# Kernel optimization log

Measured on AMD Instinct MI355X. Metric: run time of the kernel, lower is better.

## Reference

```python
import jax, jax.numpy as jnp
import numpy as np

B, T, D = 2, 2048, 1024
H, DK, DV = 16, 64, 64
DFF = 4096
CONV = 4
EPS = 1e-6


def _layernorm(x):
    # elementwise_affine=False LayerNorm
    mu = jnp.mean(x, axis=-1, keepdims=True)
    xc = x - mu
    return xc * jax.lax.rsqrt(jnp.mean(xc * xc, axis=-1, keepdims=True) + EPS)


def _l2norm(x):
    return x * jax.lax.rsqrt(jnp.sum(x * x, axis=-1, keepdims=True) + EPS)


def _modulate(x, shift, scale):
    return x * (1.0 + scale[:, None, :]) + shift[:, None, :]


def _short_conv(x, w):
    # causal depthwise conv1d (kernel CONV) + SiLU; x: [B,T,Dc], w: [Dc,CONV]
    Tn = x.shape[1]
    xp = jnp.pad(x, ((0, 0), (CONV - 1, 0), (0, 0)))
    y = xp[:, 0:Tn, :] * w[:, 0]
    for i in range(1, CONV):
        y = y + xp[:, i:i + Tn, :] * w[:, i]
    return jax.nn.silu(y)


def _delta_rule(q, k, v, beta):
    # delta-rule linear-attention recurrence (fused_recurrent form)
    # q,k: [B,T,H,DK], v: [B,T,H,DV], beta: [B,T,H]
    scale = DK ** -0.5
    qs = jnp.moveaxis(q * scale, 1, 0)
    ks = jnp.moveaxis(k, 1, 0)
    vs = jnp.moveaxis(v, 1, 0)
    bs = jnp.moveaxis(beta, 1, 0)
    S0 = jnp.zeros((q.shape[0], H, DK, DV), q.dtype)

    def step(S, inp):
        qt, kt, vt, bt = inp
        pred = jnp.einsum('bhk,bhkv->bhv', kt, S)        # k_t^T S
        delta = bt[..., None] * (vt - pred)              # beta_t (v_t - k_t^T S)
        S = S + jnp.einsum('bhk,bhv->bhkv', kt, delta)   # rank-1 delta update
        o = jnp.einsum('bhk,bhkv->bhv', qt, S)
        return S, o

    _, o = jax.lax.scan(step, S0, (qs, ks, vs, bs))
    return jnp.moveaxis(o, 0, 1)  # [B,T,H,DV]


def _deltanet(xm, Wq, Wk, Wv, Wb, wcq, wck, wcv, w_onorm, Wo):
    Bb, Tn, Dd = xm.shape
    q = _short_conv(xm @ Wq, wcq)
    k = _short_conv(xm @ Wk, wck)
    v = _short_conv(xm @ Wv, wcv)
    beta = jax.nn.sigmoid(xm @ Wb)                        # [B,T,H]
    q = _l2norm(q.reshape(Bb, Tn, H, DK))
    k = _l2norm(k.reshape(Bb, Tn, H, DK))
    v = v.reshape(Bb, Tn, H, DV)
    o = _delta_rule(q, k, v, beta)
    # per-head RMSNorm output norm
    o = o * jax.lax.rsqrt(jnp.mean(o * o, axis=-1, keepdims=True) + EPS) * w_onorm
    return o.reshape(Bb, Tn, Dd) @ Wo


def setup_inputs():
    key = jax.random.key(0)
    ks = jax.random.split(key, 20)
    s = 0.02
    return {
        "x": jax.random.normal(ks[0], (B, T, D), jnp.float32),
        "c": jax.random.normal(ks[1], (B, D), jnp.float32),
        "W_ada": jax.random.normal(ks[2], (D, 6 * D), jnp.float32) * s,
        "b_ada": jnp.zeros((6 * D,), jnp.float32),
        "Wq": jax.random.normal(ks[3], (D, H * DK), jnp.float32) * s,
        "Wk": jax.random.normal(ks[4], (D, H * DK), jnp.float32) * s,
        "Wv": jax.random.normal(ks[5], (D, H * DV), jnp.float32) * s,
        "Wb": jax.random.normal(ks[6], (D, H), jnp.float32) * s,
        "wcq": jax.random.normal(ks[7], (H * DK, CONV), jnp.float32) * 0.5,
        "wck": jax.random.normal(ks[8], (H * DK, CONV), jnp.float32) * 0.5,
        "wcv": jax.random.normal(ks[9], (H * DV, CONV), jnp.float32) * 0.5,
        "w_onorm": jnp.ones((DV,), jnp.float32),
        "Wo": jax.random.normal(ks[10], (H * DV, D), jnp.float32) * s,
        "W1": jax.random.normal(ks[11], (D, DFF), jnp.float32) * s,
        "b1": jnp.zeros((DFF,), jnp.float32),
        "W2": jax.random.normal(ks[12], (DFF, D), jnp.float32) * s,
        "b2": jnp.zeros((D,), jnp.float32),
    }


def reference(x, c, W_ada, b_ada, Wq, Wk, Wv, Wb, wcq, wck, wcv, w_onorm, Wo, W1, b1, W2, b2):
    mods = jax.nn.silu(c) @ W_ada + b_ada
    sh_a, sc_a, g_a, sh_m, sc_m, g_m = jnp.split(mods, 6, axis=-1)
    attn_out = _deltanet(_modulate(_layernorm(x), sh_a, sc_a),
                         Wq, Wk, Wv, Wb, wcq, wck, wcv, w_onorm, Wo)
    x = x + g_a[:, None, :] * attn_out
    h = _modulate(_layernorm(x), sh_m, sc_m)
    mlp = jax.nn.gelu(h @ W1 + b1, approximate=True) @ W2 + b2
    return x + g_m[:, None, :] * mlp
```

## Files before the change

### kernel.cpp

```cpp
#include <hip/hip_runtime.h>
#include <math.h>

typedef __attribute__((ext_vector_type(4))) float f32x4;
typedef __attribute__((ext_vector_type(8))) short bf16x8;
typedef __attribute__((ext_vector_type(4))) short s16x4;

__device__ __forceinline__ short f2bf(float f) {
  union { float f; unsigned u; } c; c.f = f;
  unsigned r = c.u + 0x7FFFu + ((c.u >> 16) & 1u);
  return (short)(r >> 16);
}
__device__ __forceinline__ float bf2f(short b) {
  union { unsigned u; float f; } c;
  c.u = ((unsigned)(unsigned short)b) << 16;
  return c.f;
}
__device__ __forceinline__ f32x4 mfma16(bf16x8 a, bf16x8 b, f32x4 c) {
  return __builtin_amdgcn_mfma_f32_16x16x32_bf16(a, b, c, 0, 0, 0);
}
__device__ __forceinline__ void gload16(const short* g, short* l) {
  __builtin_amdgcn_global_load_lds(
      (const __attribute__((address_space(1))) unsigned int*)g,
      (__attribute__((address_space(3))) unsigned int*)l, 16, 0, 0);
}

__global__ void k_transpose_bf16(const float* __restrict__ in, short* __restrict__ out,
                                 int K, int N) {
  __shared__ float tile[32][33];
  int n0 = blockIdx.x * 32, k0 = blockIdx.y * 32;
  int tx = threadIdx.x & 31, ty = threadIdx.x >> 5;
  for (int i = ty; i < 32; i += 8) tile[i][tx] = in[(long)(k0 + i) * N + n0 + tx];
  __syncthreads();
  for (int i = ty; i < 32; i += 8) out[(long)(n0 + i) * K + k0 + tx] = f2bf(tile[tx][i]);
}

__global__ void k_transpose_wb(const float* __restrict__ Wb, short* __restrict__ WbT) {
  int idx = blockIdx.x * 256 + threadIdx.x;
  int n = idx >> 10, k = idx & 1023;
  WbT[n * 1024 + k] = f2bf(Wb[k * 16 + n]);
}

__global__ void k_mods_p1(const float* __restrict__ c, const float* __restrict__ W_ada,
                          float* __restrict__ part) {
  int cx = blockIdx.x, dc = blockIdx.y, tid = threadIdx.x;
  __shared__ float s0[128], s1[128];
  if (tid < 128) {
    float v = c[dc * 128 + tid];
    s0[tid] = v / (1.f + expf(-v));
  } else {
    int t = tid - 128;
    float v = c[1024 + dc * 128 + t];
    s1[t] = v / (1.f + expf(-v));
  }
  __syncthreads();
  int col = cx * 256 + tid;
  float a0 = 0.f, a1 = 0.f;
  const float* wp = W_ada + (long)(dc * 128) * 6144 + col;
  for (int d = 0; d < 128; d++) {
    float w = wp[(long)d * 6144];
    a0 += s0[d] * w;
    a1 += s1[d] * w;
  }
  part[((long)dc * 2) * 6144 + col] = a0;
  part[((long)dc * 2 + 1) * 6144 + col] = a1;
}
__global__ void k_mods_p2(const float* __restrict__ part, const float* __restrict__ b_ada,
                          float* __restrict__ mods) {
  int col = blockIdx.x * 256 + threadIdx.x;
  float a0 = 0.f, a1 = 0.f;
  for (int dc = 0; dc < 8; dc++) {
    a0 += part[((long)dc * 2) * 6144 + col];
    a1 += part[((long)dc * 2 + 1) * 6144 + col];
  }
  float b = b_ada[col];
  mods[col] = a0 + b;
  mods[6144 + col] = a1 + b;
}

__global__ void k_ln_mod(const float* __restrict__ x, const float* __restrict__ mods,
                         short* __restrict__ out, int sh_off, int sc_off) {
  int row = blockIdx.x, tid = threadIdx.x, b = row >> 11;
  float4 v = ((const float4*)(x + (long)row * 1024))[tid];
  float s = v.x + v.y + v.z + v.w;
  float ss = v.x * v.x + v.y * v.y + v.z * v.z + v.w * v.w;
  #pragma unroll
  for (int off = 1; off < 64; off <<= 1) { s += __shfl_xor(s, off); ss += __shfl_xor(ss, off); }
  __shared__ float rs[4], rq[4];
  if ((tid & 63) == 0) { rs[tid >> 6] = s; rq[tid >> 6] = ss; }
  __syncthreads();
  s = rs[0] + rs[1] + rs[2] + rs[3];
  ss = rq[0] + rq[1] + rq[2] + rq[3];
  float mu = s * (1.f / 1024.f);
  float rstd = rsqrtf(ss * (1.f / 1024.f) - mu * mu + 1e-6f);
  const float* shv = mods + b * 6144 + sh_off;
  const float* scv = mods + b * 6144 + sc_off;
  int c0 = tid * 4;
  float xs[4] = {v.x, v.y, v.z, v.w};
  s16x4 ov;
  #pragma unroll
  for (int j = 0; j < 4; j++)
    ov[j] = f2bf((xs[j] - mu) * rstd * (1.f + scv[c0 + j]) + shv[c0 + j]);
  ((s16x4*)(out + (long)row * 1024))[tid] = ov;
}

__global__ __launch_bounds__(256) void k_beta_mfma(
    const short* __restrict__ xm, const short* __restrict__ WbT,
    float* __restrict__ beta) {
  int tid = threadIdx.x, w = tid >> 6, l = tid & 63;
  int lr = l & 15, lg = l >> 4;
  int row0 = blockIdx.x * 64 + w * 16;
  const short* ap = xm + (long)(row0 + lr) * 1024 + lg * 8;
  const short* bp = WbT + lr * 1024 + lg * 8;
  f32x4 acc = (f32x4){0.f, 0.f, 0.f, 0.f};
  #pragma unroll 8
  for (int kk = 0; kk < 1024; kk += 32) {
    bf16x8 a = *(const bf16x8*)(ap + kk);
    bf16x8 b = *(const bf16x8*)(bp + kk);
    acc = mfma16(a, b, acc);
  }
  #pragma unroll
  for (int i = 0; i < 4; i++) {
    int row = row0 + lg * 4 + i;
    beta[row * 16 + lr] = 1.f / (1.f + expf(-acc[i]));
  }
}

template <int NORM, int OUTBF>
__global__ void k_conv(const float* __restrict__ pre, const float* __restrict__ w,
                       void* __restrict__ out, float scale, int ldp) {
  int row = blockIdx.x, tid = threadIdx.x, t = row & 2047;
  int c0 = tid * 4;
  const float* base = pre + (long)row * ldp + c0;
  float xr[4][4];
  #pragma unroll
  for (int i = 0; i < 4; i++) {
    int tt = t - 3 + i;
    if (tt >= 0) {
      float4 xv = *(const float4*)(base + (long)(i - 3) * ldp);
      xr[i][0] = xv.x; xr[i][1] = xv.y; xr[i][2] = xv.z; xr[i][3] = xv.w;
    } else {
      xr[i][0] = xr[i][1] = xr[i][2] = xr[i][3] = 0.f;
    }
  }
  float y[4];
  #pragma unroll
  for (int j = 0; j < 4; j++) {
    float4 wv = *(const float4*)(w + (long)(c0 + j) * 4);
    float a = xr[0][j] * wv.x + xr[1][j] * wv.y + xr[2][j] * wv.z + xr[3][j] * wv.w;
    y[j] = a / (1.f + expf(-a));
  }
  if (NORM) {
    float ssq = y[0] * y[0] + y[1] * y[1] + y[2] * y[2] + y[3] * y[3];
    #pragma unroll
    for (int off = 1; off < 16; off <<= 1) ssq += __shfl_xor(ssq, off);
    float r = rsqrtf(ssq + 1e-6f) * scale;
    #pragma unroll
    for (int j = 0; j < 4; j++) y[j] *= r;
  }
  if (OUTBF) {
    s16x4 ov;
    #pragma unroll
    for (int j = 0; j < 4; j++) ov[j] = f2bf(y[j]);
    ((s16x4*)((short*)out + (long)row * 1024))[tid] = ov;
  } else {
    float4 ov = {y[0], y[1], y[2], y[3]};
    ((float4*)((float*)out + (long)row * 1024))[tid] = ov;
  }
}

__global__ __launch_bounds__(256) void k_phaseA(
    const float* __restrict__ kf, const float* __restrict__ vf,
    const short* __restrict__ qbf, const float* __restrict__ beta,
    short* __restrict__ Wc, short* __restrict__ UTc,
    short* __restrict__ Lc, short* __restrict__ KTc) {
  int chunk = blockIdx.x, chain = blockIdx.y;
  int b = chain >> 4, h = chain & 15;
  long rowbase = (long)b * 2048 + chunk * 64;
  int col0 = h * 64;
  long cb = ((long)chain * 32 + chunk) * 4096;
  __shared__ short Kb[64][72], KTb[64][72], VTb[64][72], Mb[64][72];
  __shared__ float Sf[64][65], Mf[64][65];
  __shared__ float Tl[4][16][20];
  __shared__ float bl[64];
  int tid = threadIdx.x, w = tid >> 6, l = tid & 63;
  int lr = l & 15, lg = l >> 4;

  for (int i = tid; i < 64 * 65; i += 256) (&Mf[0][0])[i] = 0.f;
  {
    int t = tid & 63, g = tid >> 6;
    if (tid < 64) bl[tid] = beta[(rowbase + tid) * 16 + h];
    #pragma unroll
    for (int i = 0; i < 4; i++) {
      int dk = g * 16 + i * 4;
      float4 kv = *(const float4*)(kf + (rowbase + t) * 1024 + col0 + dk);
      float4 vv = *(const float4*)(vf + (rowbase + t) * 1024 + col0 + dk);
      #pragma unroll
      for (int j = 0; j < 4; j++) {
        short ks = f2bf(((const float*)&kv)[j]);
        Kb[t][dk + j] = ks;
        KTb[dk + j][t] = ks;
        VTb[dk + j][t] = f2bf(((const float*)&vv)[j]);
      }
    }
  }
  __syncthreads();
  {
    bf16x8 af0 = *(const bf16x8*)&Kb[w * 16 + lr][lg * 8];
    bf16x8 af1 = *(const bf16x8*)&Kb[w * 16 + lr][32 + lg * 8];
    #pragma unroll
    for (int nt = 0; nt < 4; nt++) {
      f32x4 acc = (f32x4){0.f, 0.f, 0.f, 0.f};
      acc = mfma16(af0, *(const bf16x8*)&Kb[nt * 16 + lr][lg * 8], acc);
      acc = mfma16(af1, *(const bf16x8*)&Kb[nt * 16 + lr][32 + lg * 8], acc);
      #pragma unroll
      for (int i = 0; i < 4; i++) {
        int row = w * 16 + lg * 4 + i, col = nt * 16 + lr;
        Sf[row][col] = (col < row) ? bl[row] * acc[i] : 0.f;
      }
    }
  }
  __syncthreads();
  if (w == 0) {
    int blk = l >> 4, colc = l & 15, base = blk * 16;
    float mcol[16];
    #pragma unroll
    for (int r = 0; r < 16; r++) {
      float s = (r == colc) ? 1.f : 0.f;
      #pragma unroll
      for (int j = 0; j < 16; j++)
        if (j < r) s -= Sf[base + r][base + j] * mcol[j];
      mcol[r] = s;
    }
    #pragma unroll
    for (int r = 0; r < 16; r++) Mf[base + r][base + colc] = mcol[r];
  } else if (w <= 2) {
    int idx = (w - 1) * 64 + l;
    #pragma unroll
    for (int i = 0; i < 4; i++) {
      int v = idx * 4 + i, row = v >> 3, cg = (v & 7) * 8;
      *(bf16x8*)&KTc[cb + row * 64 + cg] = *(const bf16x8*)&KTb[row][cg];
    }
  }
  __syncthreads();
  if (w < 3) {
    int j = w;
    int r = l & 15, c4 = (l >> 4) * 4;
    for (int i = j + 1; i < 4; i++) {
      float t4[4] = {0.f, 0.f, 0.f, 0.f};
      for (int k = j; k < i; k++) {
        #pragma unroll
        for (int m = 0; m < 16; m++) {
          float a = Sf[i * 16 + r][k * 16 + m];
          #pragma unroll
          for (int ii = 0; ii < 4; ii++)
            t4[ii] += a * Mf[k * 16 + m][j * 16 + c4 + ii];
        }
      }
      #pragma unroll
      for (int ii = 0; ii < 4; ii++) Tl[w][r][c4 + ii] = t4[ii];
      float o4[4] = {0.f, 0.f, 0.f, 0.f};
      #pragma unroll
      for (int m = 0; m < 16; m++) {
        float d = Mf[i * 16 + r][i * 16 + m];
        #pragma unroll
        for (int ii = 0; ii < 4; ii++) o4[ii] += d * Tl[w][m][c4 + ii];
      }
      #pragma unroll
      for (int ii = 0; ii < 4; ii++) Mf[i * 16 + r][j * 16 + c4 + ii] = -o4[ii];
    }
  }
  __syncthreads();
  {
    int r = tid >> 2, c0 = (tid & 3) * 16;
    #pragma unroll
    for (int j2 = 0; j2 < 16; j2++)
      Mb[r][c0 + j2] = f2bf(Mf[r][c0 + j2] * bl[c0 + j2]);
  }
  __syncthreads();
  {
    bf16x8 am0 = *(const bf16x8*)&Mb[w * 16 + lr][lg * 8];
    bf16x8 am1 = *(const bf16x8*)&Mb[w * 16 + lr][32 + lg * 8];
    bf16x8 av0 = *(const bf16x8*)&VTb[w * 16 + lr][lg * 8];
    bf16x8 av1 = *(const bf16x8*)&VTb[w * 16 + lr][32 + lg * 8];
    long qoff = (rowbase + w * 16 + lr) * 1024 + col0 + lg * 8;
    bf16x8 aq0 = *(const bf16x8*)&qbf[qoff];
    bf16x8 aq1 = *(const bf16x8*)&qbf[qoff + 32];
    #pragma unroll
    for (int nt = 0; nt < 4; nt++) {
      f32x4 wa = (f32x4){0.f, 0.f, 0.f, 0.f};
      f32x4 ua = (f32x4){0.f, 0.f, 0.f, 0.f};
      f32x4 la = (f32x4){0.f, 0.f, 0.f, 0.f};
      wa = mfma16(am0, *(const bf16x8*)&KTb[nt * 16 + lr][lg * 8], wa);
      wa = mfma16(am1, *(const bf16x8*)&KTb[nt * 16 + lr][32 + lg * 8], wa);
      ua = mfma16(av0, *(const bf16x8*)&Mb[nt * 16 + lr][lg * 8], ua);
      ua = mfma16(av1, *(const bf16x8*)&Mb[nt * 16 + lr][32 + lg * 8], ua);
      la = mfma16(aq0, *(const bf16x8*)&Kb[nt * 16 + lr][lg * 8], la);
      la = mfma16(aq1, *(const bf16x8*)&Kb[nt * 16 + lr][32 + lg * 8], la);
      #pragma unroll
      for (int i = 0; i < 4; i++) {
        int row = w * 16 + lg * 4 + i, col = nt * 16 + lr;
        Wc[cb + row * 64 + col] = f2bf(wa[i]);
        UTc[cb + row * 64 + col] = f2bf(ua[i]);
        Lc[cb + row * 64 + col] = f2bf((col <= row) ? la[i] : 0.f);
      }
    }
  }
}

__global__ __launch_bounds__(256) void k_phaseB_seq(
    const short* __restrict__ Wc, const short* __restrict__ UTc,
    const short* __restrict__ KTc, short* __restrict__ STb, short* __restrict__ DTb) {
  int ds = blockIdx.x, chain = blockIdx.y;
  __shared__ short Wl[2][64][72];
  __shared__ short Kl[2][64][72];
  __shared__ short Ul[2][16][72];
  __shared__ float STf[16][68];
  __shared__ short Sb[16][72];
  __shared__ short DTl[16][72];
  int tid = threadIdx.x, w = tid >> 6, l = tid & 63;
  int lr = l & 15, lg = l >> 4;
  for (int i = tid; i < 16 * 68; i += 256) (&STf[0][0])[i] = 0.f;
  for (int i = tid; i < 16 * 72; i += 256) (&Sb[0][0])[i] = 0;
  int srow = tid >> 2, scol = (tid & 3) * 16;
  int ur = tid >> 4, uc = (tid & 15) * 4;
  bf16x8 wreg0, wreg1, kreg0, kreg1;
  s16x4 ureg;
  {
    long cb = (long)chain * 32 * 4096;
    wreg0 = *(const bf16x8*)&Wc[cb + srow * 64 + scol];
    wreg1 = *(const bf16x8*)&Wc[cb + srow * 64 + scol + 8];
    kreg0 = *(const bf16x8*)&KTc[cb + srow * 64 + scol];
    kreg1 = *(const bf16x8*)&KTc[cb + srow * 64 + scol + 8];
    ureg  = *(const s16x4*)&UTc[cb + (ds * 16 + ur) * 64 + uc];
  }
  *(bf16x8*)&Wl[0][srow][scol] = wreg0;
  *(bf16x8*)&Wl[0][srow][scol + 8] = wreg1;
  *(bf16x8*)&Kl[0][srow][scol] = kreg0;
  *(bf16x8*)&Kl[0][srow][scol + 8] = kreg1;
  *(s16x4*)&Ul[0][ur][uc] = ureg;
  __syncthreads();
  int cur = 0;
  for (int c = 0; c < 32; c++) {
    if (c + 1 < 32) {
      long cb = ((long)chain * 32 + c + 1) * 4096;
      wreg0 = *(const bf16x8*)&Wc[cb + srow * 64 + scol];
      wreg1 = *(const bf16x8*)&Wc[cb + srow * 64 + scol + 8];
      kreg0 = *(const bf16x8*)&KTc[cb + srow * 64 + scol];
      kreg1 = *(const bf16x8*)&KTc[cb + srow * 64 + scol + 8];
      ureg  = *(const s16x4*)&UTc[cb + (ds * 16 + ur) * 64 + uc];
    }
    {
      long so = (((long)chain * 32 + c) * 64 + ds * 16 + ur) * 64 + uc;
      *(s16x4*)&STb[so] = *(const s16x4*)&Sb[ur][uc];
    }
    bf16x8 afr0 = *(const bf16x8*)&Sb[lr][lg * 8];
    bf16x8 afr1 = *(const bf16x8*)&Sb[lr][32 + lg * 8];
    f32x4 dacc = (f32x4){0.f, 0.f, 0.f, 0.f};
    dacc = mfma16(afr0, *(const bf16x8*)&Wl[cur][w * 16 + lr][lg * 8], dacc);
    dacc = mfma16(afr1, *(const bf16x8*)&Wl[cur][w * 16 + lr][32 + lg * 8], dacc);
    #pragma unroll
    for (int i = 0; i < 4; i++) {
      int dv = lg * 4 + i, tt = w * 16 + lr;
      float u = bf2f(Ul[cur][dv][tt]);
      short d = f2bf(u - dacc[i]);
      DTl[dv][tt] = d;
      DTb[(((long)chain * 32 + c) * 64 + ds * 16 + dv) * 64 + tt] = d;
    }
    __syncthreads();
    bf16x8 ad0 = *(const bf16x8*)&DTl[lr][lg * 8];
    bf16x8 ad1 = *(const bf16x8*)&DTl[lr][32 + lg * 8];
    f32x4 sacc;
    #pragma unroll
    for (int i = 0; i < 4; i++) sacc[i] = STf[lg * 4 + i][w * 16 + lr];
    sacc = mfma16(ad0, *(const bf16x8*)&Kl[cur][w * 16 + lr][lg * 8], sacc);
    sacc = mfma16(ad1, *(const bf16x8*)&Kl[cur][w * 16 + lr][32 + lg * 8], sacc);
    #pragma unroll
    for (int i = 0; i < 4; i++) {
      STf[lg * 4 + i][w * 16 + lr] = sacc[i];
      Sb[lg * 4 + i][w * 16 + lr] = f2bf(sacc[i]);
    }
    __syncthreads();
    if (c + 1 < 32) {
      int nxt = cur ^ 1;
      *(bf16x8*)&Wl[nxt][srow][scol] = wreg0;
      *(bf16x8*)&Wl[nxt][srow][scol + 8] = wreg1;
      *(bf16x8*)&Kl[nxt][srow][scol] = kreg0;
      *(bf16x8*)&Kl[nxt][srow][scol + 8] = kreg1;
      *(s16x4*)&Ul[nxt][ur][uc] = ureg;
      cur = nxt;
      __syncthreads();
    }
  }
}

__global__ __launch_bounds__(256) void k_phaseBo(
    const short* __restrict__ STb, const short* __restrict__ DTb,
    const short* __restrict__ Lc, const short* __restrict__ qbf,
    const float* __restrict__ wn, short* __restrict__ on) {
  int chunk = blockIdx.x, chain = blockIdx.y;
  int b = chain >> 4, h = chain & 15;
  int tid = threadIdx.x, w = tid >> 6, l = tid & 63;
  int lr = l & 15, lg = l >> 4;
  long cb = ((long)chain * 32 + chunk) * 4096;
  long rowbase = (long)b * 2048 + chunk * 64;
  bf16x8 aq[2], alf[2];
  long qoff = (rowbase + w * 16 + lr) * 1024 + h * 64 + lg * 8;
  aq[0] = *(const bf16x8*)&qbf[qoff];
  aq[1] = *(const bf16x8*)&qbf[qoff + 32];
  alf[0] = *(const bf16x8*)&Lc[cb + (w * 16 + lr) * 64 + lg * 8];
  alf[1] = *(const bf16x8*)&Lc[cb + (w * 16 + lr) * 64 + 32 + lg * 8];
  f32x4 oacc[4];
  #pragma unroll
  for (int nt = 0; nt < 4; nt++) {
    oacc[nt] = (f32x4){0.f, 0.f, 0.f, 0.f};
    #pragma unroll
    for (int kk = 0; kk < 2; kk++) {
      bf16x8 bs = *(const bf16x8*)&STb[cb + (nt * 16 + lr) * 64 + kk * 32 + lg * 8];
      oacc[nt] = mfma16(aq[kk], bs, oacc[nt]);
      bf16x8 bd = *(const bf16x8*)&DTb[cb + (nt * 16 + lr) * 64 + kk * 32 + lg * 8];
      oacc[nt] = mfma16(alf[kk], bd, oacc[nt]);
    }
  }
  float ss[4];
  #pragma unroll
  for (int i = 0; i < 4; i++) {
    ss[i] = 0.f;
    #pragma unroll
    for (int nt = 0; nt < 4; nt++) ss[i] += oacc[nt][i] * oacc[nt][i];
  }
  #pragma unroll
  for (int off = 1; off < 16; off <<= 1) {
    #pragma unroll
    for (int i = 0; i < 4; i++) ss[i] += __shfl_xor(ss[i], off);
  }
  float rr[4];
  #pragma unroll
  for (int i = 0; i < 4; i++) rr[i] = rsqrtf(ss[i] * (1.f / 64.f) + 1e-6f);
  float wnv[4];
  #pragma unroll
  for (int nt = 0; nt < 4; nt++) wnv[nt] = wn[nt * 16 + lr];
  #pragma unroll
  for (int nt = 0; nt < 4; nt++) {
    #pragma unroll
    for (int i = 0; i < 4; i++) {
      long orow = rowbase + w * 16 + lg * 4 + i;
      on[orow * 1024 + h * 64 + nt * 16 + lr] = f2bf(oacc[nt][i] * rr[i] * wnv[nt]);
    }
  }
}

template <int EPI>
__global__ __launch_bounds__(512, 4) void k_gemm128(
    const short* __restrict__ A, const short* __restrict__ BT, void* __restrict__ C,
    int M, int N, int K,
    const float* __restrict__ P1, const float* __restrict__ P2, const float* __restrict__ P3) {
  __shared__ short As[2][128 * 64];
  __shared__ short Bs[2][128 * 64];
  int tid = threadIdx.x, w = tid >> 6, l = tid & 63;
  int lr = l & 15, lg = l >> 4;
  int wr = w >> 2, wc = w & 3;
  int nx = gridDim.x;
  int orig = blockIdx.y * nx + blockIdx.x;
  int cpx = (nx * gridDim.y) >> 3;
  int swz = (orig & 7) * cpx + (orig >> 3);
  int bx = swz % nx, by = swz / nx;
  int row0 = by * 128, col0 = bx * 128;
  int scol = ((l & 7) ^ (l >> 3)) * 8;
  const short* Ab = A + (long)(row0 + w * 8 + (l >> 3)) * K + scol;
  const short* Bb = BT + (long)(col0 + w * 8 + (l >> 3)) * K + scol;
  f32x4 acc[4][2];
  #pragma unroll
  for (int m = 0; m < 4; m++)
    #pragma unroll
    for (int n = 0; n < 2; n++) acc[m][n] = (f32x4){0.f, 0.f, 0.f, 0.f};
  int u0 = ((0 + lg) ^ (lr & 7)) * 8;
  int u1 = ((4 + lg) ^ (lr & 7)) * 8;

#define STAGE_G(buf, kt)                                                        \
  {                                                                             \
    _Pragma("unroll") for (int i = 0; i < 2; i++) {                             \
      gload16(Ab + (long)i * 64 * K + (kt), &As[buf][(i * 64 + w * 8) * 64]);   \
      gload16(Bb + (long)i * 64 * K + (kt), &Bs[buf][(i * 64 + w * 8) * 64]);   \
    }                                                                           \
  }
#define COMPUTE_G(buf)                                                          \
  {                                                                             \
    bf16x8 af[4], bv[2];                                                        \
    _Pragma("unroll") for (int m = 0; m < 4; m++)                               \
      af[m] = *(const bf16x8*)&As[buf][(wr * 64 + m * 16 + lr) * 64 + u0];      \
    _Pragma("unroll") for (int n = 0; n < 2; n++)                               \
      bv[n] = *(const bf16x8*)&Bs[buf][(wc * 32 + n * 16 + lr) * 64 + u0];      \
    _Pragma("unroll") for (int m = 0; m < 4; m++)                               \
      _Pragma("unroll") for (int n = 0; n < 2; n++)                             \
        acc[m][n] = mfma16(af[m], bv[n], acc[m][n]);                            \
    _Pragma("unroll") for (int m = 0; m < 4; m++)                               \
      af[m] = *(const bf16x8*)&As[buf][(wr * 64 + m * 16 + lr) * 64 + u1];      \
    _Pragma("unroll") for (int n = 0; n < 2; n++)                               \
      bv[n] = *(const bf16x8*)&Bs[buf][(wc * 32 + n * 16 + lr) * 64 + u1];      \
    _Pragma("unroll") for (int m = 0; m < 4; m++)                               \
      _Pragma("unroll") for (int n = 0; n < 2; n++)                             \
        acc[m][n] = mfma16(af[m], bv[n], acc[m][n]);                            \
  }

  STAGE_G(0, 0);
  __syncthreads();
  int cur = 0;
  int ktLast = K - 64;
  for (int kt = 0; kt < ktLast; kt += 64) {
    STAGE_G(cur ^ 1, kt + 64);
    COMPUTE_G(cur);
    __syncthreads();
    cur ^= 1;
  }
  COMPUTE_G(cur);
#undef STAGE_G
#undef COMPUTE_G

  #pragma unroll
  for (int m = 0; m < 4; m++) {
    #pragma unroll
    for (int n = 0; n < 2; n++) {
      int col = col0 + wc * 32 + n * 16 + lr;
      #pragma unroll
      for (int i = 0; i < 4; i++) {
        int row = row0 + wr * 64 + m * 16 + lg * 4 + i;
        float v = acc[m][n][i];
        if (EPI == 0) {
          ((float*)C)[(long)row * N + col] = v;
        } else if (EPI == 1) {
          int bb = row >> 11;
          ((float*)C)[(long)row * N + col] =
              P1[(long)row * N + col] + P2[bb * 6144 + 2048 + col] * v;
        } else if (EPI == 2) {
          float t = v + P1[col];
          float y = 1.5957691216f * (t + 0.044715f * t * t * t);
          float g = t / (1.f + __expf(-y));
          ((short*)C)[(long)row * N + col] = f2bf(g);
        } else {
          int bb = row >> 11;
          ((float*)C)[(long)row * N + col] =
              P1[(long)row * 1024 + col] + P2[bb * 6144 + 5120 + col] * (v + P3[col]);
        }
      }
    }
  }
}

#define OFF_MODS  0L
#define OFF_MODSP 49152L
#define OFF_XM    442368L
#define OFF_QKV   8830976L
#define OFF_QBF   59162624L
#define OFF_KF    67551232L
#define OFF_VF    84328448L
#define OFF_BETA  101105664L
#define OFF_WC    101367808L
#define OFF_UT    109756416L
#define OFF_LC    118145024L
#define OFF_KT    126533632L
#define OFF_ON    134922240L
#define OFF_X2    143310848L
#define OFF_WQT   160088064L
#define OFF_WKT   162185216L
#define OFF_WVT   164282368L
#define OFF_WOT   166379520L
#define OFF_W1T   168476672L
#define OFF_W2T   176865280L
#define OFF_WBT   185253888L
#define OFF_STB   OFF_QKV
#define OFF_DTB   (OFF_QKV + 8388608L)
#define OFF_M1    (OFF_QKV + 16777216L)
#define OFF_H     OFF_XM

extern "C" void kernel_launch(void* const* d_in, const int* in_sizes, int n_in,
                              void* d_out, int out_size, void* d_ws, size_t ws_size,
                              hipStream_t stream) {
  const float* x     = (const float*)d_in[0];
  const float* c     = (const float*)d_in[1];
  const float* W_ada = (const float*)d_in[2];
  const float* b_ada = (const float*)d_in[3];
  const float* Wq    = (const float*)d_in[4];
  const float* Wk    = (const float*)d_in[5];
  const float* Wv    = (const float*)d_in[6];
  const float* Wb    = (const float*)d_in[7];
  const float* wcq   = (const float*)d_in[8];
  const float* wck   = (const float*)d_in[9];
  const float* wcv   = (const float*)d_in[10];
  const float* wn    = (const float*)d_in[11];
  const float* Wo    = (const float*)d_in[12];
  const float* W1    = (const float*)d_in[13];
  const float* b1    = (const float*)d_in[14];
  const float* W2    = (const float*)d_in[15];
  const float* b2    = (const float*)d_in[16];
  float* out = (float*)d_out;
  char* ws = (char*)d_ws;

  float* mods = (float*)(ws + OFF_MODS);
  float* modp = (float*)(ws + OFF_MODSP);
  short* xm   = (short*)(ws + OFF_XM);
  float* qkv  = (float*)(ws + OFF_QKV);
  short* qbf  = (short*)(ws + OFF_QBF);
  float* kf   = (float*)(ws + OFF_KF);
  float* vf   = (float*)(ws + OFF_VF);
  float* beta = (float*)(ws + OFF_BETA);
  short* Wc   = (short*)(ws + OFF_WC);
  short* UTc  = (short*)(ws + OFF_UT);
  short* Lc   = (short*)(ws + OFF_LC);
  short* KTc  = (short*)(ws + OFF_KT);
  short* STb  = (short*)(ws + OFF_STB);
  short* DTb  = (short*)(ws + OFF_DTB);
  short* on   = (short*)(ws + OFF_ON);
  float* x2   = (float*)(ws + OFF_X2);
  short* hbuf = (short*)(ws + OFF_H);
  short* m1   = (short*)(ws + OFF_M1);
  short* WqT  = (short*)(ws + OFF_WQT);
  short* WkT  = (short*)(ws + OFF_WKT);
  short* WvT  = (short*)(ws + OFF_WVT);
  short* WoT  = (short*)(ws + OFF_WOT);
  short* W1T  = (short*)(ws + OFF_W1T);
  short* W2T  = (short*)(ws + OFF_W2T);
  short* WbT  = (short*)(ws + OFF_WBT);

  k_transpose_bf16<<<dim3(32, 32), 256, 0, stream>>>(Wq, WqT, 1024, 1024);
  k_transpose_bf16<<<dim3(32, 32), 256, 0, stream>>>(Wk, WkT, 1024, 1024);
  k_transpose_bf16<<<dim3(32, 32), 256, 0, stream>>>(Wv, WvT, 1024, 1024);
  k_transpose_bf16<<<dim3(32, 32), 256, 0, stream>>>(Wo, WoT, 1024, 1024);
  k_transpose_bf16<<<dim3(128, 32), 256, 0, stream>>>(W1, W1T, 1024, 4096);
  k_transpose_bf16<<<dim3(32, 128), 256, 0, stream>>>(W2, W2T, 4096, 1024);
  k_transpose_wb<<<64, 256, 0, stream>>>(Wb, WbT);

  k_mods_p1<<<dim3(24, 8), 256, 0, stream>>>(c, W_ada, modp);
  k_mods_p2<<<24, 256, 0, stream>>>(modp, b_ada, mods);
  k_ln_mod<<<4096, 256, 0, stream>>>(x, mods, xm, 0, 1024);

  k_gemm128<0><<<dim3(24, 32), 512, 0, stream>>>(xm, WqT, qkv, 4096, 3072, 1024,
                                                 nullptr, nullptr, nullptr);
  k_beta_mfma<<<64, 256, 0, stream>>>(xm, WbT, beta);

  k_conv<1, 1><<<4096, 256, 0, stream>>>(qkv + 0,    wcq, qbf, 0.125f, 3072);
  k_conv<1, 0><<<4096, 256, 0, stream>>>(qkv + 1024, wck, kf, 1.f, 3072);
  k_conv<0, 0><<<4096, 256, 0, stream>>>(qkv + 2048, wcv, vf, 1.f, 3072);

  k_phaseA<<<dim3(32, 32), 256, 0, stream>>>(kf, vf, qbf, beta, Wc, UTc, Lc, KTc);
  k_phaseB_seq<<<dim3(4, 32), 256, 0, stream>>>(Wc, UTc, KTc, STb, DTb);
  k_phaseBo<<<dim3(32, 32), 256, 0, stream>>>(STb, DTb, Lc, qbf, wn, on);

  k_gemm128<1><<<dim3(8, 32), 512, 0, stream>>>(on, WoT, x2, 4096, 1024, 1024,
                                                x, mods, nullptr);

  k_ln_mod<<<4096, 256, 0, stream>>>(x2, mods, hbuf, 3072, 4096);
  k_gemm128<2><<<dim3(32, 32), 512, 0, stream>>>(hbuf, W1T, m1, 4096, 4096, 1024,
                                                 b1, nullptr, nullptr);
  k_gemm128<3><<<dim3(8, 32), 512, 0, stream>>>(m1, W2T, out, 4096, 1024, 4096,
                                                x2, mods, b2);
}
```

Measured before the change: 344.3 us.

## Store QKV in bf16, fuse three conv kernels, use 256-tile GEMM for W1

The QKV projection GEMM now writes bf16 instead of fp32. A single fused conv kernel (k_conv3) processes q, k and v together and emits bf16 k and v, and phaseA loads those bf16 tensors directly with vector loads. This cuts memory traffic and launch count, at the cost of extra bf16 rounding on the pre-conv activations and on k and v. Separately, the W1 MLP GEMM moves to a new 256x256-tile kernel with lower occupancy, aiming for more data reuse per block.

```diff
diff --git a/kernel.cpp b/kernel.cpp
--- a/kernel.cpp
+++ b/kernel.cpp
@@ -125,51 +125,54 @@
   }
 }
 
-template <int NORM, int OUTBF>
-__global__ void k_conv(const float* __restrict__ pre, const float* __restrict__ w,
-                       void* __restrict__ out, float scale, int ldp) {
+__global__ __launch_bounds__(384) void k_conv3(
+    const short* __restrict__ qkv, const float* __restrict__ wcq,
+    const float* __restrict__ wck, const float* __restrict__ wcv,
+    short* __restrict__ qbf, short* __restrict__ kb, short* __restrict__ vb) {
   int row = blockIdx.x, tid = threadIdx.x, t = row & 2047;
-  int c0 = tid * 4;
-  const float* base = pre + (long)row * ldp + c0;
-  float xr[4][4];
+  int c0 = tid * 8;
+  int seg = c0 >> 10;
+  int lc = c0 & 1023;
+  const float* wseg = (seg == 0) ? wcq : (seg == 1) ? wck : wcv;
+  float xr[4][8];
   #pragma unroll
   for (int i = 0; i < 4; i++) {
     int tt = t - 3 + i;
     if (tt >= 0) {
-      float4 xv = *(const float4*)(base + (long)(i - 3) * ldp);
-      xr[i][0] = xv.x; xr[i][1] = xv.y; xr[i][2] = xv.z; xr[i][3] = xv.w;
+      bf16x8 v = *(const bf16x8*)(qkv + (long)(row - 3 + i) * 3072 + c0);
+      #pragma unroll
+      for (int j = 0; j < 8; j++) xr[i][j] = bf2f(v[j]);
     } else {
-      xr[i][0] = xr[i][1] = xr[i][2] = xr[i][3] = 0.f;
-    }
-  }
-  float y[4];
-  #pragma unroll
-  for (int j = 0; j < 4; j++) {
-    float4 wv = *(const float4*)(w + (long)(c0 + j) * 4);
+      #pragma unroll
+      for (int j = 0; j < 8; j++) xr[i][j] = 0.f;
+    }
+  }
+  float y[8];
+  #pragma unroll
+  for (int j = 0; j < 8; j++) {
+    float4 wv = *(const float4*)(wseg + (long)(lc + j) * 4);
     float a = xr[0][j] * wv.x + xr[1][j] * wv.y + xr[2][j] * wv.z + xr[3][j] * wv.w;
-    y[j] = a / (1.f + expf(-a));
-  }
-  if (NORM) {
-    float ssq = y[0] * y[0] + y[1] * y[1] + y[2] * y[2] + y[3] * y[3];
-    #pragma unroll
-    for (int off = 1; off < 16; off <<= 1) ssq += __shfl_xor(ssq, off);
-    float r = rsqrtf(ssq + 1e-6f) * scale;
-    #pragma unroll
-    for (int j = 0; j < 4; j++) y[j] *= r;
-  }
-  if (OUTBF) {
-    s16x4 ov;
-    #pragma unroll
-    for (int j = 0; j < 4; j++) ov[j] = f2bf(y[j]);
-    ((s16x4*)((short*)out + (long)row * 1024))[tid] = ov;
-  } else {
-    float4 ov = {y[0], y[1], y[2], y[3]};
-    ((float4*)((float*)out + (long)row * 1024))[tid] = ov;
-  }
+    y[j] = a / (1.f + __expf(-a));
+  }
+  if (seg < 2) {
+    float ssq = 0.f;
+    #pragma unroll
+    for (int j = 0; j < 8; j++) ssq += y[j] * y[j];
+    #pragma unroll
+    for (int off = 1; off < 8; off <<= 1) ssq += __shfl_xor(ssq, off);
+    float r = rsqrtf(ssq + 1e-6f) * ((seg == 0) ? 0.125f : 1.f);
+    #pragma unroll
+    for (int j = 0; j < 8; j++) y[j] *= r;
+  }
+  bf16x8 ov;
+  #pragma unroll
+  for (int j = 0; j < 8; j++) ov[j] = f2bf(y[j]);
+  short* outp = (seg == 0) ? qbf : (seg == 1) ? kb : vb;
+  *(bf16x8*)(outp + (long)row * 1024 + lc) = ov;
 }
 
 __global__ __launch_bounds__(256) void k_phaseA(
-    const float* __restrict__ kf, const float* __restrict__ vf,
+    const short* __restrict__ kb, const short* __restrict__ vb,
     const short* __restrict__ qbf, const float* __restrict__ beta,
     short* __restrict__ Wc, short* __restrict__ UTc,
     short* __restrict__ Lc, short* __restrict__ KTc) {
@@ -189,18 +192,19 @@
   {
     int t = tid & 63, g = tid >> 6;
     if (tid < 64) bl[tid] = beta[(rowbase + tid) * 16 + h];
-    #pragma unroll
-    for (int i = 0; i < 4; i++) {
-      int dk = g * 16 + i * 4;
-      float4 kv = *(const float4*)(kf + (rowbase + t) * 1024 + col0 + dk);
-      float4 vv = *(const float4*)(vf + (rowbase + t) * 1024 + col0 + dk);
-      #pragma unroll
-      for (int j = 0; j < 4; j++) {
-        short ks = f2bf(((const float*)&kv)[j]);
-        Kb[t][dk + j] = ks;
-        KTb[dk + j][t] = ks;
-        VTb[dk + j][t] = f2bf(((const float*)&vv)[j]);
-      }
+    int dk0 = g * 16;
+    bf16x8 kv0 = *(const bf16x8*)(kb + (rowbase + t) * 1024 + col0 + dk0);
+    bf16x8 kv1 = *(const bf16x8*)(kb + (rowbase + t) * 1024 + col0 + dk0 + 8);
+    bf16x8 vv0 = *(const bf16x8*)(vb + (rowbase + t) * 1024 + col0 + dk0);
+    bf16x8 vv1 = *(const bf16x8*)(vb + (rowbase + t) * 1024 + col0 + dk0 + 8);
+    *(bf16x8*)&Kb[t][dk0] = kv0;
+    *(bf16x8*)&Kb[t][dk0 + 8] = kv1;
+    #pragma unroll
+    for (int j = 0; j < 8; j++) {
+      KTb[dk0 + j][t] = kv0[j];
+      KTb[dk0 + 8 + j][t] = kv1[j];
+      VTb[dk0 + j][t] = vv0[j];
+      VTb[dk0 + 8 + j][t] = vv1[j];
     }
   }
   __syncthreads();
@@ -450,6 +454,28 @@
 }
 
 template <int EPI>
+__device__ __forceinline__ void gemm_epi(float v, int row, int col, int N, void* C,
+                                         const float* P1, const float* P2, const float* P3) {
+  if (EPI == 0) {
+    ((float*)C)[(long)row * N + col] = v;
+  } else if (EPI == 1) {
+    int bb = row >> 11;
+    ((float*)C)[(long)row * N + col] = P1[(long)row * N + col] + P2[bb * 6144 + 2048 + col] * v;
+  } else if (EPI == 2) {
+    float t = v + P1[col];
+    float y = 1.5957691216f * (t + 0.044715f * t * t * t);
+    float g = t / (1.f + __expf(-y));
+    ((short*)C)[(long)row * N + col] = f2bf(g);
+  } else if (EPI == 3) {
+    int bb = row >> 11;
+    ((float*)C)[(long)row * N + col] =
+        P1[(long)row * 1024 + col] + P2[bb * 6144 + 5120 + col] * (v + P3[col]);
+  } else {
+    ((short*)C)[(long)row * N + col] = f2bf(v);
+  }
+}
+
+template <int EPI>
 __global__ __launch_bounds__(512, 4) void k_gemm128(
     const short* __restrict__ A, const short* __restrict__ BT, void* __restrict__ C,
     int M, int N, int K,
@@ -517,33 +543,87 @@
 #undef COMPUTE_G
 
   #pragma unroll
-  for (int m = 0; m < 4; m++) {
+  for (int m = 0; m < 4; m++)
     #pragma unroll
     for (int n = 0; n < 2; n++) {
       int col = col0 + wc * 32 + n * 16 + lr;
       #pragma unroll
-      for (int i = 0; i < 4; i++) {
-        int row = row0 + wr * 64 + m * 16 + lg * 4 + i;
-        float v = acc[m][n][i];
-        if (EPI == 0) {
-          ((float*)C)[(long)row * N + col] = v;
-        } else if (EPI == 1) {
-          int bb = row >> 11;
-          ((float*)C)[(long)row * N + col] =
-              P1[(long)row * N + col] + P2[bb * 6144 + 2048 + col] * v;
-        } else if (EPI == 2) {
-          float t = v + P1[col];
-          float y = 1.5957691216f * (t + 0.044715f * t * t * t);
-          float g = t / (1.f + __expf(-y));
-          ((short*)C)[(long)row * N + col] = f2bf(g);
-        } else {
-          int bb = row >> 11;
-          ((float*)C)[(long)row * N + col] =
-              P1[(long)row * 1024 + col] + P2[bb * 6144 + 5120 + col] * (v + P3[col]);
-        }
-      }
-    }
-  }
+      for (int i = 0; i < 4; i++)
+        gemm_epi<EPI>(acc[m][n][i], row0 + wr * 64 + m * 16 + lg * 4 + i, col, N, C, P1, P2, P3);
+    }
+}
+
+template <int EPI>
+__global__ __launch_bounds__(512, 2) void k_gemm256(
+    const short* __restrict__ A, const short* __restrict__ BT, void* __restrict__ C,
+    int M, int N, int K,
+    const float* __restrict__ P1, const float* __restrict__ P2, const float* __restrict__ P3) {
+  __shared__ short As[2][256 * 64];
+  __shared__ short Bs[2][256 * 64];
+  int tid = threadIdx.x, w = tid >> 6, l = tid & 63;
+  int lr = l & 15, lg = l >> 4;
+  int wr = w >> 2, wc = w & 3;
+  int nx = gridDim.x;
+  int orig = blockIdx.y * nx + blockIdx.x;
+  int cpx = (nx * gridDim.y) >> 3;
+  int swz = (orig & 7) * cpx + (orig >> 3);
+  int bx = swz % nx, by = swz / nx;
+  int row0 = by * 256, col0 = bx * 256;
+  int scol = ((l & 7) ^ (l >> 3)) * 8;
+  const short* Ab = A + (long)(row0 + w * 8 + (l >> 3)) * K + scol;
+  const short* Bb = BT + (long)(col0 + w * 8 + (l >> 3)) * K + scol;
+  f32x4 acc[8][4];
+  #pragma unroll
+  for (int m = 0; m < 8; m++)
+    #pragma unroll
+    for (int n = 0; n < 4; n++) acc[m][n] = (f32x4){0.f, 0.f, 0.f, 0.f};
+  int u0 = ((0 + lg) ^ (lr & 7)) * 8;
+  int u1 = ((4 + lg) ^ (lr & 7)) * 8;
+
+#define STAGE_G2(buf, kt)                                                       \
+  {                                                                             \
+    _Pragma("unroll") for (int i = 0; i < 4; i++) {                             \
+      gload16(Ab + (long)i * 64 * K + (kt), &As[buf][(i * 64 + w * 8) * 64]);   \
+      gload16(Bb + (long)i * 64 * K + (kt), &Bs[buf][(i * 64 + w * 8) * 64]);   \
+    }                                                                           \
+  }
+#define COMPUTE_HALF2(buf, u)                                                   \
+  {                                                                             \
+    bf16x8 af[8], bv[4];                                                        \
+    _Pragma("unroll") for (int m = 0; m < 8; m++)                               \
+      af[m] = *(const bf16x8*)&As[buf][(wr * 128 + m * 16 + lr) * 64 + (u)];    \
+    _Pragma("unroll") for (int n = 0; n < 4; n++)                               \
+      bv[n] = *(const bf16x8*)&Bs[buf][(wc * 64 + n * 16 + lr) * 64 + (u)];     \
+    _Pragma("unroll") for (int m = 0; m < 8; m++)                               \
+      _Pragma("unroll") for (int n = 0; n < 4; n++)                             \
+        acc[m][n] = mfma16(af[m], bv[n], acc[m][n]);                            \
+  }
+
+  STAGE_G2(0, 0);
+  __syncthreads();
+  int cur = 0;
+  int ktLast = K - 64;
+  for (int kt = 0; kt < ktLast; kt += 64) {
+    STAGE_G2(cur ^ 1, kt + 64);
+    COMPUTE_HALF2(cur, u0);
+    COMPUTE_HALF2(cur, u1);
+    __syncthreads();
+    cur ^= 1;
+  }
+  COMPUTE_HALF2(cur, u0);
+  COMPUTE_HALF2(cur, u1);
+#undef STAGE_G2
+#undef COMPUTE_HALF2
+
+  #pragma unroll
+  for (int m = 0; m < 8; m++)
+    #pragma unroll
+    for (int n = 0; n < 4; n++) {
+      int col = col0 + wc * 64 + n * 16 + lr;
+      #pragma unroll
+      for (int i = 0; i < 4; i++)
+        gemm_epi<EPI>(acc[m][n][i], row0 + wr * 128 + m * 16 + lg * 4 + i, col, N, C, P1, P2, P3);
+    }
 }
 
 #define OFF_MODS  0L
@@ -598,10 +678,10 @@
   float* mods = (float*)(ws + OFF_MODS);
   float* modp = (float*)(ws + OFF_MODSP);
   short* xm   = (short*)(ws + OFF_XM);
-  float* qkv  = (float*)(ws + OFF_QKV);
+  short* qkv  = (short*)(ws + OFF_QKV);
   short* qbf  = (short*)(ws + OFF_QBF);
-  float* kf   = (float*)(ws + OFF_KF);
-  float* vf   = (float*)(ws + OFF_VF);
+  short* kb   = (short*)(ws + OFF_KF);
+  short* vb   = (short*)(ws + OFF_VF);
   float* beta = (float*)(ws + OFF_BETA);
   short* Wc   = (short*)(ws + OFF_WC);
   short* UTc  = (short*)(ws + OFF_UT);
@@ -633,15 +713,13 @@
   k_mods_p2<<<24, 256, 0, stream>>>(modp, b_ada, mods);
   k_ln_mod<<<4096, 256, 0, stream>>>(x, mods, xm, 0, 1024);
 
-  k_gemm128<0><<<dim3(24, 32), 512, 0, stream>>>(xm, WqT, qkv, 4096, 3072, 1024,
+  k_gemm128<4><<<dim3(24, 32), 512, 0, stream>>>(xm, WqT, qkv, 4096, 3072, 1024,
                                                  nullptr, nullptr, nullptr);
   k_beta_mfma<<<64, 256, 0, stream>>>(xm, WbT, beta);
 
-  k_conv<1, 1><<<4096, 256, 0, stream>>>(qkv + 0,    wcq, qbf, 0.125f, 3072);
-  k_conv<1, 0><<<4096, 256, 0, stream>>>(qkv + 1024, wck, kf, 1.f, 3072);
-  k_conv<0, 0><<<4096, 256, 0, stream>>>(qkv + 2048, wcv, vf, 1.f, 3072);
-
-  k_phaseA<<<dim3(32, 32), 256, 0, stream>>>(kf, vf, qbf, beta, Wc, UTc, Lc, KTc);
+  k_conv3<<<4096, 384, 0, stream>>>(qkv, wcq, wck, wcv, qbf, kb, vb);
+
+  k_phaseA<<<dim3(32, 32), 256, 0, stream>>>(kb, vb, qbf, beta, Wc, UTc, Lc, KTc);
   k_phaseB_seq<<<dim3(4, 32), 256, 0, stream>>>(Wc, UTc, KTc, STb, DTb);
   k_phaseBo<<<dim3(32, 32), 256, 0, stream>>>(STb, DTb, Lc, qbf, wn, on);
 
@@ -649,7 +727,7 @@
                                                 x, mods, nullptr);
 
   k_ln_mod<<<4096, 256, 0, stream>>>(x2, mods, hbuf, 3072, 4096);
-  k_gemm128<2><<<dim3(32, 32), 512, 0, stream>>>(hbuf, W1T, m1, 4096, 4096, 1024,
+  k_gemm256<2><<<dim3(16, 16), 512, 0, stream>>>(hbuf, W1T, m1, 4096, 4096, 1024,
                                                  b1, nullptr, nullptr);
   k_gemm128<3><<<dim3(8, 32), 512, 0, stream>>>(m1, W2T, out, 4096, 1024, 4096,
                                                 x2, mods, b2);
```

Result: faster. 327.6 us (-4.9%).
